# Kernel optimization log

Measured on AMD Instinct MI355X. Metric: run time of the kernel, lower is better.

## Reference

```python
import jax, jax.numpy as jnp
import numpy as np

NPOINT = 1024   # npoint
K = 20          # num_samples[0]


def _fps(pts, npoint):
    """Iterative furthest point sampling. pts: [N,3] -> indices [npoint] (starts at idx 0)."""
    N = pts.shape[0]

    def step(carry, _):
        min_d, last = carry
        d = jnp.sum((pts - pts[last]) ** 2, axis=-1)          # [N] dist to last selected
        min_d = jnp.minimum(min_d, d)                          # running min-dist to selected set
        nxt = jnp.argmax(min_d).astype(jnp.int32)
        return (min_d, nxt), nxt

    init = (jnp.full((N,), 1e10, pts.dtype), jnp.int32(0))
    _, rest = jax.lax.scan(step, init, None, length=npoint - 1)
    return jnp.concatenate([jnp.zeros((1,), jnp.int32), rest])


def _pdist2(q, p):
    """Squared pairwise distances. q:[M,3], p:[N,3] -> [M,N], clamped to >=0 (matches pdist2squared)."""
    d = jnp.sum(q * q, -1)[:, None] + jnp.sum(p * p, -1)[None, :] - 2.0 * (q @ p.T)
    return jnp.maximum(d, 0.0)


def _knn(q, p, k):
    """k nearest neighbors of each q among p, dropping the closest (self), ascending order."""
    d = _pdist2(q, p)                       # [M,N]
    _, idx = jax.lax.top_k(-d, k + 1)       # ascending distance order
    return idx[:, 1:]                       # drop self, [M,k]


def setup_inputs() -> dict:
    key = jax.random.key(0)
    points = jax.random.normal(key, (4, 16384, 3), dtype=jnp.float32)
    return {"points": points}


def reference(points):
    B, N, _ = points.shape
    # --- FPS node sampling (Sample module) ---
    xyz_ind = jax.vmap(lambda p: _fps(p, NPOINT))(points)                  # [B, N1]
    xyz_query = jnp.take_along_axis(points, xyz_ind[:, :, None], axis=1)  # [B, N1, 3]

    # --- Gmid: neighbors of the N1 query points among all N points ---
    nbr_mid = jax.vmap(lambda q, p: _knn(q, p, K))(xyz_query, points)      # [B, N1, K]
    src_mid = jnp.take_along_axis(points, nbr_mid.reshape(B, -1, 1), axis=1).reshape(B, NPOINT, K, 3)
    d_mid = xyz_query[:, :, None, :] - src_mid                             # edata['d'] = pos[dst]-pos[src]

    # --- Gout: neighbors among the downsampled N1 points themselves ---
    nbr_out = jax.vmap(lambda q: _knn(q, q, K))(xyz_query)                 # [B, N1, K]
    src_out = jnp.take_along_axis(xyz_query, nbr_out.reshape(B, -1, 1), axis=1).reshape(B, NPOINT, K, 3)
    d_out = xyz_query[:, :, None, :] - src_out

    return xyz_ind, xyz_query, nbr_mid, d_mid, nbr_out, d_out
```

## Files before the change

### kernel.cpp

```cpp
#include <hip/hip_runtime.h>
#include <stdint.h>

#define BATCH   4
#define NPTS    16384
#define NPOINT  1024
#define KNN     20
#define KSEL    21

typedef unsigned long long u64;

#define FPS_THREADS 512
#define PPT (NPTS / FPS_THREADS)
#define KNN_MID_BLK0 4
#define KNN_OUT_BLK0 (4 + 512)
#define GRID_BLOCKS  (4 + 512 + 512)

__device__ __forceinline__ float opaque_f(float x) {
  __asm__ volatile("" : "+v"(x));
  return x;
}

#define REPEAT32(M) \
  M(0) M(1) M(2) M(3) M(4) M(5) M(6) M(7) \
  M(8) M(9) M(10) M(11) M(12) M(13) M(14) M(15) \
  M(16) M(17) M(18) M(19) M(20) M(21) M(22) M(23) \
  M(24) M(25) M(26) M(27) M(28) M(29) M(30) M(31)

#define FPS_DECL(i) float px##i, py##i, pz##i, md##i;

#define FPS_INIT(i) { \
    int idx = (i) * FPS_THREADS + t; \
    px##i = opaque_f(P[idx * 3 + 0]); \
    py##i = opaque_f(P[idx * 3 + 1]); \
    pz##i = opaque_f(P[idx * 3 + 2]); \
    md##i = 1e10f; }

#define FPS_STEP(i) { \
    float dx = __fsub_rn(px##i, qx); \
    float dy = __fsub_rn(py##i, qy); \
    float dz = __fsub_rn(pz##i, qz); \
    float d  = __fadd_rn(__fadd_rn(__fmul_rn(dx, dx), __fmul_rn(dy, dy)), \
                         __fmul_rn(dz, dz)); \
    float m = fminf(md##i, d); \
    md##i = m; \
    bool g = (m > best); \
    best = g ? m : best; \
    bi   = g ? (i) : bi; }

__global__ __launch_bounds__(FPS_THREADS)
__attribute__((amdgpu_waves_per_eu(2, 2)))
void fused_kernel(const float* __restrict__ pts, float* __restrict__ out,
                  u64* __restrict__ slots,
                  float* __restrict__ out_nbr_mid,
                  float* __restrict__ out_d_mid,
                  float* __restrict__ out_nbr_out,
                  float* __restrict__ out_d_out) {
  if (blockIdx.x < 4) {
    __builtin_amdgcn_s_setprio(3);
    const int b = blockIdx.x;
    const float* P = pts + (size_t)b * NPTS * 3;
    float* out_ind = out;
    float* out_q   = out + BATCH * NPOINT;
    const int t = threadIdx.x;

    REPEAT32(FPS_DECL)
    REPEAT32(FPS_INIT)

    __shared__ float s_val[2][FPS_THREADS / 64];
    __shared__ int   s_idx[2][FPS_THREADS / 64];

    if (t == 0) {
      out_ind[b * NPOINT] = 0.0f;
      float ax = P[0], ay = P[1], az = P[2];
      size_t o0 = (size_t)(b * NPOINT) * 3;
      out_q[o0 + 0] = ax; out_q[o0 + 1] = ay; out_q[o0 + 2] = az;
    }
    float qx = P[0], qy = P[1], qz = P[2];

    for (int it = 1; it < NPOINT; ++it) {
      const int p = it & 1;
      float best = -1.0f;
      int bi = 0;
      REPEAT32(FPS_STEP)
      int bidx = bi * FPS_THREADS + t;

#pragma unroll
      for (int off = 32; off >= 1; off >>= 1) {
        float ov = __shfl_down(best, off);
        int   oi = __shfl_down(bidx, off);
        if (ov > best || (ov == best && oi < bidx)) { best = ov; bidx = oi; }
      }

      if ((t & 63) == 0) { s_val[p][t >> 6] = best; s_idx[p][t >> 6] = bidx; }
      __syncthreads();

      float bv = s_val[p][0];
      int   bx = s_idx[p][0];
#pragma unroll
      for (int w = 1; w < FPS_THREADS / 64; ++w) {
        float v = s_val[p][w];
        int   x = s_idx[p][w];
        if (v > bv || (v == bv && x < bx)) { bv = v; bx = x; }
      }

      qx = P[bx * 3 + 0];
      qy = P[bx * 3 + 1];
      qz = P[bx * 3 + 2];

      if (t == 0) {
        u64 pv = (u64)(unsigned)(bx | (it << 20));
        __hip_atomic_store(&slots[(size_t)it * BATCH + b], pv,
                           __ATOMIC_RELAXED, __HIP_MEMORY_SCOPE_AGENT);
        out_ind[b * NPOINT + it] = (float)bx;
        size_t o = (size_t)(b * NPOINT + it) * 3;
        out_q[o + 0] = qx; out_q[o + 1] = qy; out_q[o + 2] = qz;
      }
    }
  } else if (blockIdx.x < KNN_OUT_BLK0) {
#pragma clang fp contract(off)
    __builtin_amdgcn_s_setprio(0);
    const int kb   = blockIdx.x - KNN_MID_BLK0;
    const int wid  = kb * 8 + (threadIdx.x >> 6);
    const int lane = threadIdx.x & 63;
    const int b    = wid >> 10;
    const int qi   = wid & (NPOINT - 1);
    const float* C = pts + (size_t)b * NPTS * 3;

    int widx = 0;
    if (qi > 0) {
      const u64* sp = slots + (size_t)qi * BATCH + b;
      u64 v;
      for (;;) {
        v = __hip_atomic_load(sp, __ATOMIC_RELAXED,
                              __HIP_MEMORY_SCOPE_AGENT);
        if ((v >> 63) == 0 &&
            ((((unsigned)(v >> 20)) & 0x3FFu) == (unsigned)qi)) break;
        __builtin_amdgcn_s_sleep(32);
      }
      widx = (int)((unsigned)v & 0x3FFFu);
    }

    const float qx = C[widx * 3 + 0];
    const float qy = C[widx * 3 + 1];
    const float qz = C[widx * 3 + 2];
    const float qq = (qx * qx + qy * qy) + qz * qz;

    u64 best[KSEL];
#pragma unroll
    for (int j = 0; j < KSEL; ++j) best[j] = 0xFFFFFFFFFFFFFFFFull;

    for (int j = lane; j < NPTS; j += 64) {
      float px = C[j * 3 + 0], py = C[j * 3 + 1], pz = C[j * 3 + 2];
      float pp  = (px * px + py * py) + pz * pz;
      float dot = __builtin_fmaf(qz, pz, __builtin_fmaf(qy, py, qx * px));
      float d = (qq + pp) - 2.0f * dot;
      d = fmaxf(d, 0.0f);
      u64 key = ((u64)__float_as_uint(d) << 32) | (unsigned)j;
      if (key < best[KSEL - 1]) {
        u64 c = key;
#pragma unroll
        for (int s = 0; s < KSEL; ++s) {
          u64 o = best[s];
          bool l = c < o;
          u64 nb = l ? c : o;
          c = l ? o : c;
          best[s] = nb;
        }
      }
    }

    int hp = 1;
    u64 head = best[0];
    int myK = -1, myIdx = 0;
#pragma unroll
    for (int r = 0; r < KSEL; ++r) {
      u64 v = head; int src = lane;
#pragma unroll
      for (int off = 32; off >= 1; off >>= 1) {
        u64 ov = __shfl_down(v, off);
        int os = __shfl_down(src, off);
        if (ov < v) { v = ov; src = os; }
      }
      v   = __shfl(v, 0);
      src = __shfl(src, 0);
      if (r >= 1 && lane == r - 1) {
        myIdx = (int)(unsigned)(v & 0xFFFFFFFFull);
        myK = r - 1;
      }
      if (lane == src) {
        u64 h = 0xFFFFFFFFFFFFFFFFull;
#pragma unroll
        for (int s = 1; s < KSEL; ++s) if (hp == s) h = best[s];
        head = h;
        hp++;
      }
    }

    if (myK >= 0) {
      size_t o = (size_t)(b * NPOINT + qi) * KNN + myK;
      out_nbr_mid[o] = (float)myIdx;
      float sx = C[myIdx * 3 + 0], sy = C[myIdx * 3 + 1],
            sz = C[myIdx * 3 + 2];
      out_d_mid[o * 3 + 0] = qx - sx;
      out_d_mid[o * 3 + 1] = qy - sy;
      out_d_mid[o * 3 + 2] = qz - sz;
    }
  } else {
#pragma clang fp contract(off)
    __builtin_amdgcn_s_setprio(0);
    const int kb   = blockIdx.x - KNN_OUT_BLK0;
    const int wid  = kb * 8 + (threadIdx.x >> 6);
    const int lane = threadIdx.x & 63;
    const int b    = wid >> 10;
    const int qi   = wid & (NPOINT - 1);
    const float* C = pts + (size_t)b * NPTS * 3;

    int wq = 0;
    if (qi > 0) {
      const u64* sp = slots + (size_t)qi * BATCH + b;
      u64 v;
      for (;;) {
        v = __hip_atomic_load(sp, __ATOMIC_RELAXED,
                              __HIP_MEMORY_SCOPE_AGENT);
        if ((v >> 63) == 0 &&
            ((((unsigned)(v >> 20)) & 0x3FFu) == (unsigned)qi)) break;
        __builtin_amdgcn_s_sleep(32);
      }
      wq = (int)((unsigned)v & 0x3FFFu);
    }
    const float qx = C[wq * 3 + 0];
    const float qy = C[wq * 3 + 1];
    const float qz = C[wq * 3 + 2];
    const float qq = (qx * qx + qy * qy) + qz * qz;

    int wj[NPOINT / 64];
#pragma unroll
    for (int u = 0; u < NPOINT / 64; ++u) {
      int j = u * 64 + lane;
      int w = 0;
      if (j > 0) {
        const u64* sp = slots + (size_t)j * BATCH + b;
        u64 v;
        for (;;) {
          v = __hip_atomic_load(sp, __ATOMIC_RELAXED,
                                __HIP_MEMORY_SCOPE_AGENT);
          if ((v >> 63) == 0 &&
              ((((unsigned)(v >> 20)) & 0x3FFu) == (unsigned)j)) break;
          __builtin_amdgcn_s_sleep(64);
        }
        w = (int)((unsigned)v & 0x3FFFu);
      }
      wj[u] = w;
    }

    u64 best[KSEL];
#pragma unroll
    for (int j = 0; j < KSEL; ++j) best[j] = 0xFFFFFFFFFFFFFFFFull;

#pragma unroll
    for (int u = 0; u < NPOINT / 64; ++u) {
      int j = u * 64 + lane;
      int w = wj[u];
      float px = C[w * 3 + 0], py = C[w * 3 + 1], pz = C[w * 3 + 2];
      float pp  = (px * px + py * py) + pz * pz;
      float dot = __builtin_fmaf(qz, pz, __builtin_fmaf(qy, py, qx * px));
      float d = (qq + pp) - 2.0f * dot;
      d = fmaxf(d, 0.0f);
      u64 key = ((u64)__float_as_uint(d) << 32) | (unsigned)j;
      if (key < best[KSEL - 1]) {
        u64 c = key;
#pragma unroll
        for (int s = 0; s < KSEL; ++s) {
          u64 o = best[s];
          bool l = c < o;
          u64 nb = l ? c : o;
          c = l ? o : c;
          best[s] = nb;
        }
      }
    }

    int hp = 1;
    u64 head = best[0];
    int myK = -1, myIdx = 0;
#pragma unroll
    for (int r = 0; r < KSEL; ++r) {
      u64 v = head; int src = lane;
#pragma unroll
      for (int off = 32; off >= 1; off >>= 1) {
        u64 ov = __shfl_down(v, off);
        int os = __shfl_down(src, off);
        if (ov < v) { v = ov; src = os; }
      }
      v   = __shfl(v, 0);
      src = __shfl(src, 0);
      if (r >= 1 && lane == r - 1) {
        myIdx = (int)(unsigned)(v & 0xFFFFFFFFull);
        myK = r - 1;
      }
      if (lane == src) {
        u64 h = 0xFFFFFFFFFFFFFFFFull;
#pragma unroll
        for (int s = 1; s < KSEL; ++s) if (hp == s) h = best[s];
        head = h;
        hp++;
      }
    }

    if (myK >= 0) {
      size_t o = (size_t)(b * NPOINT + qi) * KNN + myK;
      out_nbr_out[o] = (float)myIdx;
      int w = 0;
      if (myIdx > 0) {
        u64 v = __hip_atomic_load(slots + (size_t)myIdx * BATCH + b,
                                  __ATOMIC_RELAXED, __HIP_MEMORY_SCOPE_AGENT);
        w = (int)((unsigned)v & 0x3FFFu);
      }
      float sx = C[w * 3 + 0], sy = C[w * 3 + 1], sz = C[w * 3 + 2];
      out_d_out[o * 3 + 0] = qx - sx;
      out_d_out[o * 3 + 1] = qy - sy;
      out_d_out[o * 3 + 2] = qz - sz;
    }
  }
}

extern "C" void kernel_launch(void* const* d_in, const int* in_sizes, int n_in,
                              void* d_out, int out_size, void* d_ws,
                              size_t ws_size, hipStream_t stream) {
  (void)in_sizes; (void)n_in; (void)out_size; (void)ws_size;
  const float* pts = (const float*)d_in[0];
  float* out = (float*)d_out;

  u64* slots = (u64*)d_ws;

  float* out_nbr_mid = out + (size_t)BATCH * NPOINT * 4;
  float* out_d_mid   = out_nbr_mid + (size_t)BATCH * NPOINT * KNN;
  float* out_nbr_out = out_d_mid + (size_t)BATCH * NPOINT * KNN * 3;
  float* out_d_out   = out_nbr_out + (size_t)BATCH * NPOINT * KNN;

  hipLaunchKernelGGL(fused_kernel, dim3(GRID_BLOCKS), dim3(FPS_THREADS), 0,
                     stream, pts, out, slots,
                     out_nbr_mid, out_d_mid, out_nbr_out, out_d_out);
}
```

Baseline: 2.573 ms.

## Split fused FPS/KNN kernel into two sequential launches without spin-wait slots

Replaces the single fused kernel, where KNN blocks poll atomically published FPS results, with a separate FPS kernel followed by a KNN kernel. Slots become plain int indices and all polling loops and sleeps are removed. This eliminates spin-wait traffic and contention with the latency-critical FPS blocks, and lets the KNN kernel request higher occupancy. In exchange it gives up overlapping KNN work with the serial FPS loop.

Result: slower. 2.739 ms (+6.5%).

```diff
diff --git a/kernel.cpp b/kernel.cpp
--- a/kernel.cpp
+++ b/kernel.cpp
@@ -11,9 +11,6 @@
 
 #define FPS_THREADS 512
 #define PPT (NPTS / FPS_THREADS)
-#define KNN_MID_BLK0 4
-#define KNN_OUT_BLK0 (4 + 512)
-#define GRID_BLOCKS  (4 + 512 + 512)
 
 __device__ __forceinline__ float opaque_f(float x) {
   __asm__ volatile("" : "+v"(x));
@@ -49,96 +46,86 @@
 
 __global__ __launch_bounds__(FPS_THREADS)
 __attribute__((amdgpu_waves_per_eu(2, 2)))
-void fused_kernel(const float* __restrict__ pts, float* __restrict__ out,
-                  u64* __restrict__ slots,
-                  float* __restrict__ out_nbr_mid,
-                  float* __restrict__ out_d_mid,
-                  float* __restrict__ out_nbr_out,
-                  float* __restrict__ out_d_out) {
-  if (blockIdx.x < 4) {
-    __builtin_amdgcn_s_setprio(3);
-    const int b = blockIdx.x;
-    const float* P = pts + (size_t)b * NPTS * 3;
-    float* out_ind = out;
-    float* out_q   = out + BATCH * NPOINT;
-    const int t = threadIdx.x;
-
-    REPEAT32(FPS_DECL)
-    REPEAT32(FPS_INIT)
-
-    __shared__ float s_val[2][FPS_THREADS / 64];
-    __shared__ int   s_idx[2][FPS_THREADS / 64];
+void fps_kernel(const float* __restrict__ pts, float* __restrict__ out,
+                int* __restrict__ slots) {
+  const int b = blockIdx.x;
+  const float* P = pts + (size_t)b * NPTS * 3;
+  float* out_ind = out;
+  float* out_q   = out + BATCH * NPOINT;
+  const int t = threadIdx.x;
+
+  REPEAT32(FPS_DECL)
+  REPEAT32(FPS_INIT)
+
+  __shared__ float s_val[2][FPS_THREADS / 64];
+  __shared__ int   s_idx[2][FPS_THREADS / 64];
+
+  if (t == 0) {
+    out_ind[b * NPOINT] = 0.0f;
+    slots[b * NPOINT] = 0;
+    float ax = P[0], ay = P[1], az = P[2];
+    size_t o0 = (size_t)(b * NPOINT) * 3;
+    out_q[o0 + 0] = ax; out_q[o0 + 1] = ay; out_q[o0 + 2] = az;
+  }
+  float qx = P[0], qy = P[1], qz = P[2];
+
+  for (int it = 1; it < NPOINT; ++it) {
+    const int p = it & 1;
+    float best = -1.0f;
+    int bi = 0;
+    REPEAT32(FPS_STEP)
+    int bidx = bi * FPS_THREADS + t;
+
+#pragma unroll
+    for (int off = 32; off >= 1; off >>= 1) {
+      float ov = __shfl_down(best, off);
+      int   oi = __shfl_down(bidx, off);
+      if (ov > best || (ov == best && oi < bidx)) { best = ov; bidx = oi; }
+    }
+
+    if ((t & 63) == 0) { s_val[p][t >> 6] = best; s_idx[p][t >> 6] = bidx; }
+    __syncthreads();
+
+    float bv = s_val[p][0];
+    int   bx = s_idx[p][0];
+#pragma unroll
+    for (int w = 1; w < FPS_THREADS / 64; ++w) {
+      float v = s_val[p][w];
+      int   x = s_idx[p][w];
+      if (v > bv || (v == bv && x < bx)) { bv = v; bx = x; }
+    }
+
+    qx = P[bx * 3 + 0];
+    qy = P[bx * 3 + 1];
+    qz = P[bx * 3 + 2];
 
     if (t == 0) {
-      out_ind[b * NPOINT] = 0.0f;
-      float ax = P[0], ay = P[1], az = P[2];
-      size_t o0 = (size_t)(b * NPOINT) * 3;
-      out_q[o0 + 0] = ax; out_q[o0 + 1] = ay; out_q[o0 + 2] = az;
-    }
-    float qx = P[0], qy = P[1], qz = P[2];
-
-    for (int it = 1; it < NPOINT; ++it) {
-      const int p = it & 1;
-      float best = -1.0f;
-      int bi = 0;
-      REPEAT32(FPS_STEP)
-      int bidx = bi * FPS_THREADS + t;
-
-#pragma unroll
-      for (int off = 32; off >= 1; off >>= 1) {
-        float ov = __shfl_down(best, off);
-        int   oi = __shfl_down(bidx, off);
-        if (ov > best || (ov == best && oi < bidx)) { best = ov; bidx = oi; }
-      }
-
-      if ((t & 63) == 0) { s_val[p][t >> 6] = best; s_idx[p][t >> 6] = bidx; }
-      __syncthreads();
-
-      float bv = s_val[p][0];
-      int   bx = s_idx[p][0];
-#pragma unroll
-      for (int w = 1; w < FPS_THREADS / 64; ++w) {
-        float v = s_val[p][w];
-        int   x = s_idx[p][w];
-        if (v > bv || (v == bv && x < bx)) { bv = v; bx = x; }
-      }
-
-      qx = P[bx * 3 + 0];
-      qy = P[bx * 3 + 1];
-      qz = P[bx * 3 + 2];
-
-      if (t == 0) {
-        u64 pv = (u64)(unsigned)(bx | (it << 20));
-        __hip_atomic_store(&slots[(size_t)it * BATCH + b], pv,
-                           __ATOMIC_RELAXED, __HIP_MEMORY_SCOPE_AGENT);
-        out_ind[b * NPOINT + it] = (float)bx;
-        size_t o = (size_t)(b * NPOINT + it) * 3;
-        out_q[o + 0] = qx; out_q[o + 1] = qy; out_q[o + 2] = qz;
-      }
-    }
-  } else if (blockIdx.x < KNN_OUT_BLK0) {
+      slots[b * NPOINT + it] = bx;
+      out_ind[b * NPOINT + it] = (float)bx;
+      size_t o = (size_t)(b * NPOINT + it) * 3;
+      out_q[o + 0] = qx; out_q[o + 1] = qy; out_q[o + 2] = qz;
+    }
+  }
+}
+
+__global__ __launch_bounds__(FPS_THREADS)
+__attribute__((amdgpu_waves_per_eu(4)))
+void knn_kernel(const float* __restrict__ pts,
+                const int* __restrict__ slots,
+                float* __restrict__ out_nbr_mid,
+                float* __restrict__ out_d_mid,
+                float* __restrict__ out_nbr_out,
+                float* __restrict__ out_d_out) {
+  if (blockIdx.x < 512) {
 #pragma clang fp contract(off)
-    __builtin_amdgcn_s_setprio(0);
-    const int kb   = blockIdx.x - KNN_MID_BLK0;
+    const int kb   = blockIdx.x;
     const int wid  = kb * 8 + (threadIdx.x >> 6);
     const int lane = threadIdx.x & 63;
     const int b    = wid >> 10;
     const int qi   = wid & (NPOINT - 1);
     const float* C = pts + (size_t)b * NPTS * 3;
 
-    int widx = 0;
-    if (qi > 0) {
-      const u64* sp = slots + (size_t)qi * BATCH + b;
-      u64 v;
-      for (;;) {
-        v = __hip_atomic_load(sp, __ATOMIC_RELAXED,
-                              __HIP_MEMORY_SCOPE_AGENT);
-        if ((v >> 63) == 0 &&
-            ((((unsigned)(v >> 20)) & 0x3FFu) == (unsigned)qi)) break;
-        __builtin_amdgcn_s_sleep(32);
-      }
-      widx = (int)((unsigned)v & 0x3FFFu);
-    }
+    const int widx = slots[b * NPOINT + qi];
 
     const float qx = C[widx * 3 + 0];
     const float qy = C[widx * 3 + 1];
@@ -207,27 +194,14 @@
     }
   } else {
 #pragma clang fp contract(off)
-    __builtin_amdgcn_s_setprio(0);
-    const int kb   = blockIdx.x - KNN_OUT_BLK0;
+    const int kb   = blockIdx.x - 512;
     const int wid  = kb * 8 + (threadIdx.x >> 6);
     const int lane = threadIdx.x & 63;
     const int b    = wid >> 10;
     const int qi   = wid & (NPOINT - 1);
     const float* C = pts + (size_t)b * NPTS * 3;
 
-    int wq = 0;
-    if (qi > 0) {
-      const u64* sp = slots + (size_t)qi * BATCH + b;
-      u64 v;
-      for (;;) {
-        v = __hip_atomic_load(sp, __ATOMIC_RELAXED,
-                              __HIP_MEMORY_SCOPE_AGENT);
-        if ((v >> 63) == 0 &&
-            ((((unsigned)(v >> 20)) & 0x3FFu) == (unsigned)qi)) break;
-        __builtin_amdgcn_s_sleep(32);
-      }
-      wq = (int)((unsigned)v & 0x3FFFu);
-    }
+    const int wq = slots[b * NPOINT + qi];
     const float qx = C[wq * 3 + 0];
     const float qy = C[wq * 3 + 1];
     const float qz = C[wq * 3 + 2];
@@ -236,21 +210,7 @@
     int wj[NPOINT / 64];
 #pragma unroll
     for (int u = 0; u < NPOINT / 64; ++u) {
-      int j = u * 64 + lane;
-      int w = 0;
-      if (j > 0) {
-        const u64* sp = slots + (size_t)j * BATCH + b;
-        u64 v;
-        for (;;) {
-          v = __hip_atomic_load(sp, __ATOMIC_RELAXED,
-                                __HIP_MEMORY_SCOPE_AGENT);
-          if ((v >> 63) == 0 &&
-              ((((unsigned)(v >> 20)) & 0x3FFu) == (unsigned)j)) break;
-          __builtin_amdgcn_s_sleep(64);
-        }
-        w = (int)((unsigned)v & 0x3FFFu);
-      }
-      wj[u] = w;
+      wj[u] = slots[b * NPOINT + u * 64 + lane];
     }
 
     u64 best[KSEL];
@@ -310,12 +270,7 @@
     if (myK >= 0) {
       size_t o = (size_t)(b * NPOINT + qi) * KNN + myK;
       out_nbr_out[o] = (float)myIdx;
-      int w = 0;
-      if (myIdx > 0) {
-        u64 v = __hip_atomic_load(slots + (size_t)myIdx * BATCH + b,
-                                  __ATOMIC_RELAXED, __HIP_MEMORY_SCOPE_AGENT);
-        w = (int)((unsigned)v & 0x3FFFu);
-      }
+      const int w = slots[b * NPOINT + myIdx];
       float sx = C[w * 3 + 0], sy = C[w * 3 + 1], sz = C[w * 3 + 2];
       out_d_out[o * 3 + 0] = qx - sx;
       out_d_out[o * 3 + 1] = qy - sy;
@@ -331,14 +286,16 @@
   const float* pts = (const float*)d_in[0];
   float* out = (float*)d_out;
 
-  u64* slots = (u64*)d_ws;
+  int* slots = (int*)d_ws;
 
   float* out_nbr_mid = out + (size_t)BATCH * NPOINT * 4;
   float* out_d_mid   = out_nbr_mid + (size_t)BATCH * NPOINT * KNN;
   float* out_nbr_out = out_d_mid + (size_t)BATCH * NPOINT * KNN * 3;
   float* out_d_out   = out_nbr_out + (size_t)BATCH * NPOINT * KNN;
 
-  hipLaunchKernelGGL(fused_kernel, dim3(GRID_BLOCKS), dim3(FPS_THREADS), 0,
-                     stream, pts, out, slots,
-                     out_nbr_mid, out_d_mid, out_nbr_out, out_d_out);
+  hipLaunchKernelGGL(fps_kernel, dim3(BATCH), dim3(FPS_THREADS), 0, stream,
+                     pts, out, slots);
+  hipLaunchKernelGGL(knn_kernel, dim3(1024), dim3(FPS_THREADS), 0, stream,
+                     pts, slots, out_nbr_mid, out_d_mid, out_nbr_out,
+                     out_d_out);
 }
```
